# Performance work log

Hardware: AMD Instinct MI355X
Metric: run time of the kernel (lower is better)

The kernel has to match this reference:

```python
import jax, jax.numpy as jnp
import numpy as np

L, B, S, D, W = 3, 32, 512, 512, 3
EPS = 1e-6

def setup_inputs() -> dict:
    key = jax.random.key(0)
    ks = jax.random.split(key, 12)
    s = 1.0 / np.sqrt(D)
    def n(k, shape, scale=1.0):
        return jax.random.normal(k, shape, dtype=jnp.float32) * scale
    return {
        'x': n(ks[0], (B, S, D)),
        'fwd_pad': n(ks[1], (L, W, D), s),
        'bwd_pad': n(ks[2], (L, W, D), s),
        'fwd_w': n(ks[3], (L, W + 1)),
        'bwd_w': n(ks[4], (L, W + 1)),
        'fwd_w1': n(ks[5], (L, D, D), s),
        'fwd_b1': jnp.zeros((L, D), jnp.float32),
        'fwd_w2': n(ks[6], (L, D, D), s),
        'fwd_b2': jnp.zeros((L, D), jnp.float32),
        'fwd_g': jnp.ones((L, D), jnp.float32),
        'fwd_beta': jnp.zeros((L, D), jnp.float32),
        'bwd_w1': n(ks[7], (L, D, D), s),
        'bwd_b1': jnp.zeros((L, D), jnp.float32),
        'bwd_w2': n(ks[8], (L, D, D), s),
        'bwd_b2': jnp.zeros((L, D), jnp.float32),
        'bwd_g': jnp.ones((L, D), jnp.float32),
        'bwd_beta': jnp.zeros((L, D), jnp.float32),
    }

def _ln(y, g, b):
    # Annotated-transformer LayerNorm: a2*(x-mean)/(std+eps)+b2, unbiased std
    m = y.mean(-1, keepdims=True)
    sd = jnp.std(y, -1, keepdims=True, ddof=1)
    return g * (y - m) / (sd + EPS) + b

def _ffn(y, w1, b1, w2, b2):
    h = jax.nn.relu(jnp.einsum('bsd,de->bse', y, w1) + b1)
    return jnp.einsum('bse,ef->bsf', h, w2) + b2

def _wsum(padded, w, seq_len, offset):
    # weighted sum over a sliding window of width W+1 (dropout=0, eval mode)
    win = jnp.stack([padded[:, offset + k: offset + k + seq_len] for k in range(W + 1)], 0)
    return jnp.einsum('k,kbsd->bsd', w, win)

def reference(x, fwd_pad, bwd_pad, fwd_w, bwd_w,
              fwd_w1, fwd_b1, fwd_w2, fwd_b2, fwd_g, fwd_beta,
              bwd_w1, bwd_b1, bwd_w2, bwd_b2, bwd_g, bwd_beta):
    bsz, seq_len, _ = x.shape
    xf, xb = x, x
    outs = []
    for i in range(L):
        fp = jnp.broadcast_to(fwd_pad[i], (bsz, W, D))
        bp = jnp.broadcast_to(bwd_pad[i], (bsz, W, D))
        pf = jnp.concatenate([fp, xf, bp], axis=1)  # [B, S+2W, D]
        pb = jnp.concatenate([fp, xb, bp], axis=1)
        yf = _wsum(pf, fwd_w[i], seq_len, 0)       # windows [t, t+W]
        yb = _wsum(pb, bwd_w[i], seq_len, W)       # windows [t+W, t+2W]
        xf = yf + _ffn(_ln(yf, fwd_g[i], fwd_beta[i]), fwd_w1[i], fwd_b1[i], fwd_w2[i], fwd_b2[i])
        xb = yb + _ffn(_ln(yb, bwd_g[i], bwd_beta[i]), bwd_w1[i], bwd_b1[i], bwd_w2[i], bwd_b2[i])
        outs.append(jnp.concatenate([xf, xb], axis=-1))
    return jnp.stack(outs, 0)  # [L, B, S, 2D]
```

## Files before the change

### kernel.cpp

```cpp
#include <hip/hip_runtime.h>

#define S_LEN 512
#define D_DIM 512
#define BATCH 32
#define M_ROWS (BATCH * S_LEN)
#define NLAYER 3

typedef unsigned short ushort_t;
typedef __bf16 bf16_t;
typedef bf16_t bf16x8 __attribute__((ext_vector_type(8)));
typedef unsigned short u16x8 __attribute__((ext_vector_type(8)));
typedef float f32x4 __attribute__((ext_vector_type(4)));

typedef const __attribute__((address_space(1))) unsigned int* gptr_t;
typedef __attribute__((address_space(3))) unsigned int* lptr_t;

__device__ __forceinline__ ushort_t f2bf(float f) {
  unsigned u = __float_as_uint(f);
  unsigned r = (u + 0x7fffu + ((u >> 16) & 1u)) >> 16;
  return (ushort_t)r;
}

__global__ __launch_bounds__(256)
void wprep_kernel(const float* __restrict__ fw1, const float* __restrict__ fw2,
                  const float* __restrict__ bw1, const float* __restrict__ bw2,
                  ushort_t* __restrict__ wt1, ushort_t* __restrict__ wt2) {
  int z = blockIdx.z;
  int l = z >> 2, m = z & 3;
  const float* bases[4] = {fw1, fw2, bw1, bw2};
  const float* src = bases[m] + (size_t)l * D_DIM * D_DIM;
  int streamIdx = m >> 1;
  int which = m & 1;
  ushort_t* dst = (which ? wt2 : wt1) + ((size_t)streamIdx * NLAYER + l) * D_DIM * D_DIM;

  __shared__ float tile[32][33];
  int n0 = blockIdx.x * 32, k0 = blockIdx.y * 32;
  int tx = threadIdx.x, ty = threadIdx.y;
#pragma unroll
  for (int i = 0; i < 32; i += 8)
    tile[ty + i][tx] = src[(size_t)(k0 + ty + i) * D_DIM + n0 + tx];
  __syncthreads();
#pragma unroll
  for (int i = 0; i < 32; i += 8)
    dst[(size_t)(n0 + ty + i) * D_DIM + k0 + tx] = f2bf(tile[tx][ty + i]);
}

__global__ __launch_bounds__(256)
void conv_ln_kernel(const float* __restrict__ srcF, int strideF,
                    const float* __restrict__ srcB, int strideB,
                    const float* __restrict__ padLo, const float* __restrict__ padHi,
                    const float* __restrict__ wF, const float* __restrict__ wB,
                    const float* __restrict__ gF, const float* __restrict__ beF,
                    const float* __restrict__ gB, const float* __restrict__ beB,
                    ushort_t* __restrict__ yln) {
  int z = blockIdx.y;
  int tid = threadIdx.x;
  int lane = tid & 63;
  int rl = tid >> 6;
  int row = blockIdx.x * 4 + rl;
  int t = row & (S_LEN - 1);
  const float* src = z ? srcB : srcF;
  int stride = z ? strideB : strideF;
  const float* wv = z ? wB : wF;
  const float* gv = z ? gB : gF;
  const float* bv = z ? beB : beF;
  int toff = z ? 0 : -3;
  int c0 = lane * 4, c1 = 256 + lane * 4;

  float4 a0 = make_float4(0.f, 0.f, 0.f, 0.f);
  float4 a1 = make_float4(0.f, 0.f, 0.f, 0.f);
#pragma unroll
  for (int k = 0; k < 4; ++k) {
    int tt = t + k + toff;
    const float* rp;
    if (tt < 0)            rp = padLo + (size_t)(tt + 3) * D_DIM;
    else if (tt >= S_LEN)  rp = padHi + (size_t)(tt - S_LEN) * D_DIM;
    else                   rp = src + (size_t)(row + k + toff) * stride;
    float wk = wv[k];
    float4 u0 = *(const float4*)(rp + c0);
    float4 u1 = *(const float4*)(rp + c1);
    a0.x = fmaf(wk, u0.x, a0.x); a0.y = fmaf(wk, u0.y, a0.y);
    a0.z = fmaf(wk, u0.z, a0.z); a0.w = fmaf(wk, u0.w, a0.w);
    a1.x = fmaf(wk, u1.x, a1.x); a1.y = fmaf(wk, u1.y, a1.y);
    a1.z = fmaf(wk, u1.z, a1.z); a1.w = fmaf(wk, u1.w, a1.w);
  }
  float s = a0.x + a0.y + a0.z + a0.w + a1.x + a1.y + a1.z + a1.w;
#pragma unroll
  for (int o = 32; o; o >>= 1) s += __shfl_xor(s, o);
  float mean = s * (1.0f / 512.0f);
  float q = 0.f, dx;
  dx = a0.x - mean; q = fmaf(dx, dx, q);
  dx = a0.y - mean; q = fmaf(dx, dx, q);
  dx = a0.z - mean; q = fmaf(dx, dx, q);
  dx = a0.w - mean; q = fmaf(dx, dx, q);
  dx = a1.x - mean; q = fmaf(dx, dx, q);
  dx = a1.y - mean; q = fmaf(dx, dx, q);
  dx = a1.z - mean; q = fmaf(dx, dx, q);
  dx = a1.w - mean; q = fmaf(dx, dx, q);
#pragma unroll
  for (int o = 32; o; o >>= 1) q += __shfl_xor(q, o);
  float sd = sqrtf(q * (1.0f / 511.0f));
  float inv = 1.0f / (sd + 1e-6f);

  size_t base = ((size_t)z * M_ROWS + row) * D_DIM;
  float4 g0 = *(const float4*)(gv + c0), g1 = *(const float4*)(gv + c1);
  float4 b0 = *(const float4*)(bv + c0), b1 = *(const float4*)(bv + c1);
  ushort_t p0[4], p1[4];
  p0[0] = f2bf(g0.x * ((a0.x - mean) * inv) + b0.x);
  p0[1] = f2bf(g0.y * ((a0.y - mean) * inv) + b0.y);
  p0[2] = f2bf(g0.z * ((a0.z - mean) * inv) + b0.z);
  p0[3] = f2bf(g0.w * ((a0.w - mean) * inv) + b0.w);
  p1[0] = f2bf(g1.x * ((a1.x - mean) * inv) + b1.x);
  p1[1] = f2bf(g1.y * ((a1.y - mean) * inv) + b1.y);
  p1[2] = f2bf(g1.z * ((a1.z - mean) * inv) + b1.z);
  p1[3] = f2bf(g1.w * ((a1.w - mean) * inv) + b1.w);
  *(uint2*)(yln + base + c0) = *(uint2*)p0;
  *(uint2*)(yln + base + c1) = *(uint2*)p1;
}

template <int EPI>
__global__ __launch_bounds__(256)
void gemm_kernel(const ushort_t* __restrict__ A,
                 const ushort_t* __restrict__ Bt_f, const ushort_t* __restrict__ Bt_b,
                 const float* __restrict__ bias_f, const float* __restrict__ bias_b,
                 ushort_t* __restrict__ Hout,
                 float* __restrict__ Cout,
                 const float* __restrict__ srcF, const float* __restrict__ srcB,
                 int srcStride,
                 const float* __restrict__ padLo, const float* __restrict__ padHi,
                 const float* __restrict__ wF, const float* __restrict__ wB) {
  const int K = 512;
  int lin = blockIdx.x;
  int xcd = lin & 7;
  int slot = lin >> 3;
  int nblk = slot & 3;
  int G = xcd * 32 + (slot >> 2);
  int z = G >> 7;
  int mblk = G & 127;

  const ushort_t* Ab = A + (size_t)z * M_ROWS * K + (size_t)mblk * 128 * K;
  const ushort_t* Bb = (z ? Bt_b : Bt_f) + (size_t)nblk * 128 * K;

  __shared__ __attribute__((aligned(16))) ushort_t As[128 * 32];
  __shared__ __attribute__((aligned(16))) ushort_t Bs[128 * 32];

  int tid = threadIdx.x, lane = tid & 63, wave = tid >> 6;
  int wr = wave >> 1, wc = wave & 1;
  int lm = lane & 15, lq = lane >> 4;

  f32x4 acc[4][4] = {};

  for (int kb = 0; kb < 16; ++kb) {
    int k0 = kb * 32;
#pragma unroll
    for (int i = 0; i < 2; ++i) {
      int slot2 = i * 256 + tid;
      int row = slot2 >> 2, kc = slot2 & 3;
      const ushort_t* ga = Ab + (size_t)row * K + k0 + kc * 8;
      const ushort_t* gb = Bb + (size_t)row * K + k0 + kc * 8;
      __builtin_amdgcn_global_load_lds((gptr_t)(const void*)ga,
                                       (lptr_t)(void*)(As + slot2 * 8), 16, 0, 0);
      __builtin_amdgcn_global_load_lds((gptr_t)(const void*)gb,
                                       (lptr_t)(void*)(Bs + slot2 * 8), 16, 0, 0);
    }
    __syncthreads();
    bf16x8 a[4], b[4];
#pragma unroll
    for (int i = 0; i < 4; ++i) {
      union { u16x8 u; bf16x8 b; } ua, ub;
      ua.u = *(const u16x8*)&As[(wr * 64 + i * 16 + lm) * 32 + lq * 8];
      ub.u = *(const u16x8*)&Bs[(wc * 64 + i * 16 + lm) * 32 + lq * 8];
      a[i] = ua.b; b[i] = ub.b;
    }
#pragma unroll
    for (int i = 0; i < 4; ++i)
#pragma unroll
      for (int j = 0; j < 4; ++j)
        acc[i][j] = __builtin_amdgcn_mfma_f32_16x16x32_bf16(a[i], b[j], acc[i][j], 0, 0, 0);
    __syncthreads();
  }

  const float* bias = z ? bias_b : bias_f;
  if (EPI == 1) {
    ushort_t* Hb = Hout + (size_t)z * M_ROWS * 512;
#pragma unroll
    for (int i = 0; i < 4; ++i) {
      int mbase = mblk * 128 + wr * 64 + i * 16 + lq * 4;
#pragma unroll
      for (int j = 0; j < 4; ++j) {
        int n = nblk * 128 + wc * 64 + j * 16 + lm;
        float bvn = bias[n];
#pragma unroll
        for (int r = 0; r < 4; ++r) {
          float v = fmaxf(acc[i][j][r] + bvn, 0.0f);
          Hb[(size_t)(mbase + r) * 512 + n] = f2bf(v);
        }
      }
    }
  } else {
    const float* src = z ? srcB : srcF;
    const float* wv = z ? wB : wF;
    int toff = z ? 0 : -3;
    float w0 = wv[0], w1 = wv[1], w2 = wv[2], w3 = wv[3];
    float* Cb = Cout + (size_t)z * 512;
#pragma unroll
    for (int i = 0; i < 4; ++i) {
      int mbase = mblk * 128 + wr * 64 + i * 16 + lq * 4;
      int t0 = mbase & (S_LEN - 1);
      int rb = mbase - t0;
      const float* rp[7];
#pragma unroll
      for (int q = 0; q < 7; ++q) {
        int tt = t0 + toff + q;
        rp[q] = (tt < 0)       ? padLo + (size_t)(tt + 3) * D_DIM
              : (tt >= S_LEN)  ? padHi + (size_t)(tt - S_LEN) * D_DIM
                               : src + (size_t)(rb + tt) * srcStride;
      }
#pragma unroll
      for (int j = 0; j < 4; ++j) {
        int n = nblk * 128 + wc * 64 + j * 16 + lm;
        float v[7];
#pragma unroll
        for (int q = 0; q < 7; ++q) v[q] = rp[q][n];
        float bvn = bias[n];
#pragma unroll
        for (int r = 0; r < 4; ++r) {
          float y = w0 * v[r] + w1 * v[r + 1] + w2 * v[r + 2] + w3 * v[r + 3];
          Cb[(size_t)(mbase + r) * 1024 + n] = acc[i][j][r] + bvn + y;
        }
      }
    }
  }
}

extern "C" void kernel_launch(void* const* d_in, const int* in_sizes, int n_in,
                              void* d_out, int out_size, void* d_ws, size_t ws_size,
                              hipStream_t stream) {
  const float* x        = (const float*)d_in[0];
  const float* fwd_pad  = (const float*)d_in[1];
  const float* bwd_pad  = (const float*)d_in[2];
  const float* fwd_w    = (const float*)d_in[3];
  const float* bwd_w    = (const float*)d_in[4];
  const float* fwd_w1   = (const float*)d_in[5];
  const float* fwd_b1   = (const float*)d_in[6];
  const float* fwd_w2   = (const float*)d_in[7];
  const float* fwd_b2   = (const float*)d_in[8];
  const float* fwd_g    = (const float*)d_in[9];
  const float* fwd_beta = (const float*)d_in[10];
  const float* bwd_w1   = (const float*)d_in[11];
  const float* bwd_b1   = (const float*)d_in[12];
  const float* bwd_w2   = (const float*)d_in[13];
  const float* bwd_b2   = (const float*)d_in[14];
  const float* bwd_g    = (const float*)d_in[15];
  const float* bwd_beta = (const float*)d_in[16];
  float* out = (float*)d_out;

  const size_t WSZ = (size_t)D_DIM * D_DIM;
  ushort_t* wt1 = (ushort_t*)d_ws;
  ushort_t* wt2 = wt1 + 2 * NLAYER * WSZ;
  ushort_t* yln = wt2 + 2 * NLAYER * WSZ;
  ushort_t* h   = yln + (size_t)2 * M_ROWS * D_DIM;

  wprep_kernel<<<dim3(16, 16, 12), dim3(32, 8), 0, stream>>>(
      fwd_w1, fwd_w2, bwd_w1, bwd_w2, wt1, wt2);

  for (int l = 0; l < NLAYER; ++l) {
    const float *srcF, *srcB;
    int str;
    if (l == 0) {
      srcF = x; srcB = x; str = 512;
    } else {
      srcF = out + (size_t)(l - 1) * M_ROWS * 1024;
      srcB = srcF + 512;
      str = 1024;
    }
    const float* pLo = fwd_pad + (size_t)l * 3 * D_DIM;
    const float* pHi = bwd_pad + (size_t)l * 3 * D_DIM;

    conv_ln_kernel<<<dim3(M_ROWS / 4, 2), 256, 0, stream>>>(
        srcF, str, srcB, str, pLo, pHi,
        fwd_w + l * 4, bwd_w + l * 4,
        fwd_g + l * D_DIM, fwd_beta + l * D_DIM,
        bwd_g + l * D_DIM, bwd_beta + l * D_DIM,
        yln);

    gemm_kernel<1><<<1024, 256, 0, stream>>>(
        yln, wt1 + (size_t)l * WSZ, wt1 + (size_t)(NLAYER + l) * WSZ,
        fwd_b1 + l * D_DIM, bwd_b1 + l * D_DIM,
        h, nullptr,
        nullptr, nullptr, 0, nullptr, nullptr, nullptr, nullptr);

    gemm_kernel<2><<<1024, 256, 0, stream>>>(
        h, wt2 + (size_t)l * WSZ, wt2 + (size_t)(NLAYER + l) * WSZ,
        fwd_b2 + l * D_DIM, bwd_b2 + l * D_DIM,
        nullptr, out + (size_t)l * M_ROWS * 1024,
        srcF, srcB, str, pLo, pHi,
        fwd_w + l * 4, bwd_w + l * 4);
  }
}
```

Measured before the change: 518.7 us.

## Fuse FFN GEMMs into one kernel keeping hidden activations in LDS

Replaces the two separate GEMM launches (W1+ReLU writing H to global, then W2 with conv residual epilogue) with one MLP kernel. Each block owns 64 rows and processes the hidden dimension in 128-wide chunks, storing the ReLU output in XOR-swizzled shared memory and accumulating the second GEMM into registers. This removes the global round trip of the bf16 hidden tensor and one launch per layer. In exchange, tiles are smaller (64 rows), the A tile is reloaded four times, the grid drops to 512 blocks, and the 128-wide-per-wave output accumulator increases register pressure.

Result: slower. 641.1 us (+23.6%).

```diff
diff --git a/kernel.cpp b/kernel.cpp
--- a/kernel.cpp
+++ b/kernel.cpp
@@ -118,116 +118,154 @@
   *(uint2*)(yln + base + c1) = *(uint2*)p1;
 }
 
-template <int EPI>
-__global__ __launch_bounds__(256)
-void gemm_kernel(const ushort_t* __restrict__ A,
-                 const ushort_t* __restrict__ Bt_f, const ushort_t* __restrict__ Bt_b,
-                 const float* __restrict__ bias_f, const float* __restrict__ bias_b,
-                 ushort_t* __restrict__ Hout,
-                 float* __restrict__ Cout,
-                 const float* __restrict__ srcF, const float* __restrict__ srcB,
-                 int srcStride,
-                 const float* __restrict__ padLo, const float* __restrict__ padHi,
-                 const float* __restrict__ wF, const float* __restrict__ wB) {
-  const int K = 512;
-  int lin = blockIdx.x;
-  int xcd = lin & 7;
-  int slot = lin >> 3;
-  int nblk = slot & 3;
-  int G = xcd * 32 + (slot >> 2);
-  int z = G >> 7;
-  int mblk = G & 127;
-
-  const ushort_t* Ab = A + (size_t)z * M_ROWS * K + (size_t)mblk * 128 * K;
-  const ushort_t* Bb = (z ? Bt_b : Bt_f) + (size_t)nblk * 128 * K;
-
-  __shared__ __attribute__((aligned(16))) ushort_t As[128 * 32];
-  __shared__ __attribute__((aligned(16))) ushort_t Bs[128 * 32];
-
-  int tid = threadIdx.x, lane = tid & 63, wave = tid >> 6;
-  int wr = wave >> 1, wc = wave & 1;
+__global__ __launch_bounds__(256, 2)
+void mlp_kernel(const ushort_t* __restrict__ A,
+                const ushort_t* __restrict__ W1t_f, const ushort_t* __restrict__ W1t_b,
+                const ushort_t* __restrict__ W2t_f, const ushort_t* __restrict__ W2t_b,
+                const float* __restrict__ b1_f, const float* __restrict__ b1_b,
+                const float* __restrict__ b2_f, const float* __restrict__ b2_b,
+                float* __restrict__ Cout,
+                const float* __restrict__ srcF, const float* __restrict__ srcB,
+                int srcStride,
+                const float* __restrict__ padLo, const float* __restrict__ padHi,
+                const float* __restrict__ wF, const float* __restrict__ wB) {
+  int bid = blockIdx.x;
+  int z = bid & 1;
+  int mtile = bid >> 1;
+  int row0 = mtile * 64;
+
+  const ushort_t* Ab  = A + ((size_t)z * M_ROWS + row0) * 512;
+  const ushort_t* W1t = z ? W1t_b : W1t_f;
+  const ushort_t* W2t = z ? W2t_b : W2t_f;
+  const float* b1 = z ? b1_b : b1_f;
+  const float* b2 = z ? b2_b : b2_f;
+
+  __shared__ __attribute__((aligned(16))) ushort_t As[64 * 32];
+  __shared__ __attribute__((aligned(16))) ushort_t Ws[512 * 32];
+  __shared__ __attribute__((aligned(16))) ushort_t Hs[64 * 128];
+
+  int tid = threadIdx.x, lane = tid & 63, w = tid >> 6;
   int lm = lane & 15, lq = lane >> 4;
 
-  f32x4 acc[4][4] = {};
-
-  for (int kb = 0; kb < 16; ++kb) {
-    int k0 = kb * 32;
-#pragma unroll
-    for (int i = 0; i < 2; ++i) {
-      int slot2 = i * 256 + tid;
-      int row = slot2 >> 2, kc = slot2 & 3;
-      const ushort_t* ga = Ab + (size_t)row * K + k0 + kc * 8;
-      const ushort_t* gb = Bb + (size_t)row * K + k0 + kc * 8;
-      __builtin_amdgcn_global_load_lds((gptr_t)(const void*)ga,
-                                       (lptr_t)(void*)(As + slot2 * 8), 16, 0, 0);
-      __builtin_amdgcn_global_load_lds((gptr_t)(const void*)gb,
-                                       (lptr_t)(void*)(Bs + slot2 * 8), 16, 0, 0);
-    }
+  f32x4 oacc[4][8] = {};
+
+  for (int c = 0; c < 4; ++c) {
+    f32x4 hacc[4][2] = {};
+    for (int ks = 0; ks < 16; ++ks) {
+      int k0 = ks * 32;
+      {
+        int rowa = tid >> 2, ka = (tid & 3) * 8;
+        __builtin_amdgcn_global_load_lds(
+            (gptr_t)(const void*)(Ab + (size_t)rowa * 512 + k0 + ka),
+            (lptr_t)(void*)(As + tid * 8), 16, 0, 0);
+      }
+#pragma unroll
+      for (int u = 0; u < 2; ++u) {
+        int ch = u * 256 + tid;
+        int rw = ch >> 2, kw = (ch & 3) * 8;
+        __builtin_amdgcn_global_load_lds(
+            (gptr_t)(const void*)(W1t + (size_t)(c * 128 + rw) * 512 + k0 + kw),
+            (lptr_t)(void*)(Ws + ch * 8), 16, 0, 0);
+      }
+      __syncthreads();
+      bf16x8 a[4], b[2];
+#pragma unroll
+      for (int i = 0; i < 4; ++i) {
+        union { u16x8 u; bf16x8 b; } ua;
+        ua.u = *(const u16x8*)&As[(i * 16 + lm) * 32 + lq * 8];
+        a[i] = ua.b;
+      }
+#pragma unroll
+      for (int j = 0; j < 2; ++j) {
+        union { u16x8 u; bf16x8 b; } ub;
+        ub.u = *(const u16x8*)&Ws[(w * 32 + j * 16 + lm) * 32 + lq * 8];
+        b[j] = ub.b;
+      }
+#pragma unroll
+      for (int i = 0; i < 4; ++i)
+#pragma unroll
+        for (int j = 0; j < 2; ++j)
+          hacc[i][j] = __builtin_amdgcn_mfma_f32_16x16x32_bf16(a[i], b[j], hacc[i][j], 0, 0, 0);
+      __syncthreads();
+    }
+#pragma unroll
+    for (int i = 0; i < 4; ++i)
+#pragma unroll
+      for (int j = 0; j < 2; ++j) {
+        int col = w * 32 + j * 16 + lm;
+        float bv = b1[c * 128 + col];
+#pragma unroll
+        for (int r = 0; r < 4; ++r) {
+          int rowh = i * 16 + lq * 4 + r;
+          float v = fmaxf(hacc[i][j][r] + bv, 0.0f);
+          int q = (rowh * 256 + col * 2) ^ ((rowh & 7) << 4);
+          *(ushort_t*)((char*)Hs + q) = f2bf(v);
+        }
+      }
     __syncthreads();
-    bf16x8 a[4], b[4];
-#pragma unroll
-    for (int i = 0; i < 4; ++i) {
-      union { u16x8 u; bf16x8 b; } ua, ub;
-      ua.u = *(const u16x8*)&As[(wr * 64 + i * 16 + lm) * 32 + lq * 8];
-      ub.u = *(const u16x8*)&Bs[(wc * 64 + i * 16 + lm) * 32 + lq * 8];
-      a[i] = ua.b; b[i] = ub.b;
-    }
-#pragma unroll
-    for (int i = 0; i < 4; ++i)
-#pragma unroll
-      for (int j = 0; j < 4; ++j)
-        acc[i][j] = __builtin_amdgcn_mfma_f32_16x16x32_bf16(a[i], b[j], acc[i][j], 0, 0, 0);
-    __syncthreads();
+    for (int ks = 0; ks < 4; ++ks) {
+#pragma unroll
+      for (int u = 0; u < 8; ++u) {
+        int ch = u * 256 + tid;
+        int rw = ch >> 2, kw = (ch & 3) * 8;
+        __builtin_amdgcn_global_load_lds(
+            (gptr_t)(const void*)(W2t + (size_t)rw * 512 + c * 128 + ks * 32 + kw),
+            (lptr_t)(void*)(Ws + ch * 8), 16, 0, 0);
+      }
+      __syncthreads();
+      bf16x8 a[4], b[8];
+#pragma unroll
+      for (int i = 0; i < 4; ++i) {
+        int rowh = i * 16 + lm;
+        int q = (rowh * 256 + ks * 64 + lq * 16) ^ ((rowh & 7) << 4);
+        union { u16x8 u; bf16x8 b; } ua;
+        ua.u = *(const u16x8*)((const char*)Hs + q);
+        a[i] = ua.b;
+      }
+#pragma unroll
+      for (int j = 0; j < 8; ++j) {
+        union { u16x8 u; bf16x8 b; } ub;
+        ub.u = *(const u16x8*)&Ws[(w * 128 + j * 16 + lm) * 32 + lq * 8];
+        b[j] = ub.b;
+      }
+#pragma unroll
+      for (int i = 0; i < 4; ++i)
+#pragma unroll
+        for (int j = 0; j < 8; ++j)
+          oacc[i][j] = __builtin_amdgcn_mfma_f32_16x16x32_bf16(a[i], b[j], oacc[i][j], 0, 0, 0);
+      __syncthreads();
+    }
   }
 
-  const float* bias = z ? bias_b : bias_f;
-  if (EPI == 1) {
-    ushort_t* Hb = Hout + (size_t)z * M_ROWS * 512;
-#pragma unroll
-    for (int i = 0; i < 4; ++i) {
-      int mbase = mblk * 128 + wr * 64 + i * 16 + lq * 4;
-#pragma unroll
-      for (int j = 0; j < 4; ++j) {
-        int n = nblk * 128 + wc * 64 + j * 16 + lm;
-        float bvn = bias[n];
-#pragma unroll
-        for (int r = 0; r < 4; ++r) {
-          float v = fmaxf(acc[i][j][r] + bvn, 0.0f);
-          Hb[(size_t)(mbase + r) * 512 + n] = f2bf(v);
-        }
-      }
-    }
-  } else {
-    const float* src = z ? srcB : srcF;
-    const float* wv = z ? wB : wF;
-    int toff = z ? 0 : -3;
-    float w0 = wv[0], w1 = wv[1], w2 = wv[2], w3 = wv[3];
-    float* Cb = Cout + (size_t)z * 512;
-#pragma unroll
-    for (int i = 0; i < 4; ++i) {
-      int mbase = mblk * 128 + wr * 64 + i * 16 + lq * 4;
-      int t0 = mbase & (S_LEN - 1);
-      int rb = mbase - t0;
-      const float* rp[7];
-#pragma unroll
-      for (int q = 0; q < 7; ++q) {
-        int tt = t0 + toff + q;
-        rp[q] = (tt < 0)       ? padLo + (size_t)(tt + 3) * D_DIM
-              : (tt >= S_LEN)  ? padHi + (size_t)(tt - S_LEN) * D_DIM
-                               : src + (size_t)(rb + tt) * srcStride;
-      }
-#pragma unroll
-      for (int j = 0; j < 4; ++j) {
-        int n = nblk * 128 + wc * 64 + j * 16 + lm;
-        float v[7];
-#pragma unroll
-        for (int q = 0; q < 7; ++q) v[q] = rp[q][n];
-        float bvn = bias[n];
-#pragma unroll
-        for (int r = 0; r < 4; ++r) {
-          float y = w0 * v[r] + w1 * v[r + 1] + w2 * v[r + 2] + w3 * v[r + 3];
-          Cb[(size_t)(mbase + r) * 1024 + n] = acc[i][j][r] + bvn + y;
-        }
+  const float* src = z ? srcB : srcF;
+  const float* wv = z ? wB : wF;
+  int toff = z ? 0 : -3;
+  float w0 = wv[0], w1 = wv[1], w2 = wv[2], w3 = wv[3];
+  float* Cb = Cout + (size_t)z * 512;
+#pragma unroll
+  for (int i = 0; i < 4; ++i) {
+    int mbase = row0 + i * 16 + lq * 4;
+    int t0 = mbase & (S_LEN - 1);
+    int rb = mbase - t0;
+    const float* rp[7];
+#pragma unroll
+    for (int q = 0; q < 7; ++q) {
+      int tt = t0 + toff + q;
+      rp[q] = (tt < 0)       ? padLo + (size_t)(tt + 3) * D_DIM
+            : (tt >= S_LEN)  ? padHi + (size_t)(tt - S_LEN) * D_DIM
+                             : src + (size_t)(rb + tt) * srcStride;
+    }
+#pragma unroll
+    for (int j = 0; j < 8; ++j) {
+      int n = w * 128 + j * 16 + lm;
+      float v[7];
+#pragma unroll
+      for (int q = 0; q < 7; ++q) v[q] = rp[q][n];
+      float bvn = b2[n];
+#pragma unroll
+      for (int r = 0; r < 4; ++r) {
+        float y = w0 * v[r] + w1 * v[r + 1] + w2 * v[r + 2] + w3 * v[r + 3];
+        Cb[(size_t)(mbase + r) * 1024 + n] = oacc[i][j][r] + bvn + y;
       }
     }
   }
@@ -259,7 +297,6 @@
   ushort_t* wt1 = (ushort_t*)d_ws;
   ushort_t* wt2 = wt1 + 2 * NLAYER * WSZ;
   ushort_t* yln = wt2 + 2 * NLAYER * WSZ;
-  ushort_t* h   = yln + (size_t)2 * M_ROWS * D_DIM;
 
   wprep_kernel<<<dim3(16, 16, 12), dim3(32, 8), 0, stream>>>(
       fwd_w1, fwd_w2, bwd_w1, bwd_w2, wt1, wt2);
@@ -284,16 +321,13 @@
         bwd_g + l * D_DIM, bwd_beta + l * D_DIM,
         yln);
 
-    gemm_kernel<1><<<1024, 256, 0, stream>>>(
-        yln, wt1 + (size_t)l * WSZ, wt1 + (size_t)(NLAYER + l) * WSZ,
+    mlp_kernel<<<512, 256, 0, stream>>>(
+        yln,
+        wt1 + (size_t)l * WSZ, wt1 + (size_t)(NLAYER + l) * WSZ,
+        wt2 + (size_t)l * WSZ, wt2 + (size_t)(NLAYER + l) * WSZ,
         fwd_b1 + l * D_DIM, bwd_b1 + l * D_DIM,
-        h, nullptr,
-        nullptr, nullptr, 0, nullptr, nullptr, nullptr, nullptr);
-
-    gemm_kernel<2><<<1024, 256, 0, stream>>>(
-        h, wt2 + (size_t)l * WSZ, wt2 + (size_t)(NLAYER + l) * WSZ,
         fwd_b2 + l * D_DIM, bwd_b2 + l * D_DIM,
-        nullptr, out + (size_t)l * M_ROWS * 1024,
+        out + (size_t)l * M_ROWS * 1024,
         srcF, srcB, str, pLo, pHi,
         fwd_w + l * 4, bwd_w + l * 4);
   }
```

## Rewrite FFN GEMMs as 256x256 tiles with double-buffered swizzled LDS pipeline

Applied to the files above, without the earlier changes.

Replaces the 128x128, single-buffered GEMM with 256x256 tiles per 512-thread block, a K-step of 64, and double-buffered LDS. Global-to-LDS staging of later K slices is interleaved with MFMA phases, using s_setprio, explicit vmcnt waits and barriers. LDS rows use an XOR swizzle to avoid bank conflicts. This aims to hide load latency and raise MFMA utilisation and operand reuse, but the grid shrinks to 256 blocks, which leaves some CUs idle or underfilled on a 256-CU part, and register pressure rises.

After: 490.4 us. 5.5% less time.

```diff
diff --git a/kernel.cpp b/kernel.cpp
--- a/kernel.cpp
+++ b/kernel.cpp
@@ -118,81 +118,185 @@
   *(uint2*)(yln + base + c1) = *(uint2*)p1;
 }
 
+#define PHASE_PRE()                                         \
+  __builtin_amdgcn_sched_barrier(0);                        \
+  __builtin_amdgcn_s_barrier();                             \
+  asm volatile("s_waitcnt lgkmcnt(0)" ::: "memory");        \
+  __builtin_amdgcn_sched_barrier(0);                        \
+  __builtin_amdgcn_s_setprio(1);
+
+#define PHASE_PRE_NOLGKM()                                  \
+  __builtin_amdgcn_sched_barrier(0);                        \
+  __builtin_amdgcn_s_barrier();                             \
+  __builtin_amdgcn_s_setprio(1);
+
+#define PHASE_POST()                                        \
+  __builtin_amdgcn_s_setprio(0);                            \
+  __builtin_amdgcn_sched_barrier(0);                        \
+  __builtin_amdgcn_s_barrier();
+
+#define GROUP_END_CK4()                                     \
+  __builtin_amdgcn_s_setprio(0);                            \
+  __builtin_amdgcn_sched_barrier(0);                        \
+  asm volatile("s_waitcnt vmcnt(4)" ::: "memory");          \
+  __builtin_amdgcn_sched_barrier(0);                        \
+  __builtin_amdgcn_s_barrier();
+
+#define GROUP_END_CK0()                                     \
+  __builtin_amdgcn_s_setprio(0);                            \
+  __builtin_amdgcn_sched_barrier(0);                        \
+  asm volatile("s_waitcnt vmcnt(0)" ::: "memory");          \
+  __builtin_amdgcn_sched_barrier(0);                        \
+  __builtin_amdgcn_s_barrier();
+
+#define READ_A(MH)                                                        \
+  _Pragma("unroll")                                                       \
+  for (int m_ = 0; m_ < 4; ++m_) {                                        \
+    _Pragma("unroll")                                                     \
+    for (int kk_ = 0; kk_ < 2; ++kk_) {                                   \
+      int row_ = ((MH) * 4 + m_) * 32 + wr16lm;                           \
+      int idx_ = (row_ * 64 + kk_ * 32 + lq * 8) ^ ((row_ & 7) * 8);      \
+      union { u16x8 u; bf16x8 b; } t_;                                    \
+      t_.u = *(const u16x8*)&pa[idx_];                                    \
+      aF[kk_][m_] = t_.b;                                                 \
+    }                                                                     \
+  }
+
+#define READ_B(NH)                                                        \
+  _Pragma("unroll")                                                       \
+  for (int n_ = 0; n_ < 2; ++n_) {                                        \
+    _Pragma("unroll")                                                     \
+    for (int kk_ = 0; kk_ < 2; ++kk_) {                                   \
+      int row_ = ((NH) * 2 + n_) * 64 + wc16lm;                           \
+      int idx_ = (row_ * 64 + kk_ * 32 + lq * 8) ^ ((row_ & 7) * 8);      \
+      union { u16x8 u; bf16x8 b; } t_;                                    \
+      t_.u = *(const u16x8*)&pb[idx_];                                    \
+      bF[NH][kk_][n_] = t_.b;                                             \
+    }                                                                     \
+  }
+
+#define MFMA16(MH, NH)                                                    \
+  _Pragma("unroll")                                                       \
+  for (int kk_ = 0; kk_ < 2; ++kk_)                                       \
+    _Pragma("unroll")                                                     \
+    for (int m_ = 0; m_ < 4; ++m_)                                        \
+      _Pragma("unroll")                                                   \
+      for (int n_ = 0; n_ < 2; ++n_)                                      \
+        acc[(MH) * 4 + m_][(NH) * 2 + n_] =                               \
+            __builtin_amdgcn_mfma_f32_16x16x32_bf16(                      \
+                aF[kk_][m_], bF[NH][kk_][n_],                             \
+                acc[(MH) * 4 + m_][(NH) * 2 + n_], 0, 0, 0);
+
 template <int EPI>
-__global__ __launch_bounds__(256)
-void gemm_kernel(const ushort_t* __restrict__ A,
-                 const ushort_t* __restrict__ Bt_f, const ushort_t* __restrict__ Bt_b,
-                 const float* __restrict__ bias_f, const float* __restrict__ bias_b,
-                 ushort_t* __restrict__ Hout,
-                 float* __restrict__ Cout,
-                 const float* __restrict__ srcF, const float* __restrict__ srcB,
-                 int srcStride,
-                 const float* __restrict__ padLo, const float* __restrict__ padHi,
-                 const float* __restrict__ wF, const float* __restrict__ wB) {
+__global__ __launch_bounds__(512, 2)
+void gemm256_kernel(const ushort_t* __restrict__ A,
+                    const ushort_t* __restrict__ Bt_f, const ushort_t* __restrict__ Bt_b,
+                    const float* __restrict__ bias_f, const float* __restrict__ bias_b,
+                    ushort_t* __restrict__ Hout,
+                    float* __restrict__ Cout,
+                    const float* __restrict__ srcF, const float* __restrict__ srcB,
+                    int srcStride,
+                    const float* __restrict__ padLo, const float* __restrict__ padHi,
+                    const float* __restrict__ wF, const float* __restrict__ wB) {
   const int K = 512;
-  int lin = blockIdx.x;
-  int xcd = lin & 7;
-  int slot = lin >> 3;
-  int nblk = slot & 3;
-  int G = xcd * 32 + (slot >> 2);
+  int bid = blockIdx.x;
+  int G = (bid & 7) * 32 + (bid >> 3);
   int z = G >> 7;
-  int mblk = G & 127;
-
-  const ushort_t* Ab = A + (size_t)z * M_ROWS * K + (size_t)mblk * 128 * K;
-  const ushort_t* Bb = (z ? Bt_b : Bt_f) + (size_t)nblk * 128 * K;
-
-  __shared__ __attribute__((aligned(16))) ushort_t As[128 * 32];
-  __shared__ __attribute__((aligned(16))) ushort_t Bs[128 * 32];
+  int t2 = G & 127;
+  int mblk = t2 >> 1, nblk = t2 & 1;
+  int row0 = mblk * 256, n0 = nblk * 256;
+
+  const ushort_t* Ab = A + (size_t)z * M_ROWS * K + (size_t)row0 * K;
+  const ushort_t* Bb = (z ? Bt_b : Bt_f) + (size_t)n0 * K;
+
+  __shared__ __attribute__((aligned(16))) ushort_t As[2][256 * 64];
+  __shared__ __attribute__((aligned(16))) ushort_t Bs[2][256 * 64];
 
   int tid = threadIdx.x, lane = tid & 63, wave = tid >> 6;
-  int wr = wave >> 1, wc = wave & 1;
+  int wr = wave >> 2, wc = wave & 3;
   int lm = lane & 15, lq = lane >> 4;
-
-  f32x4 acc[4][4] = {};
-
-  for (int kb = 0; kb < 16; ++kb) {
-    int k0 = kb * 32;
-#pragma unroll
-    for (int i = 0; i < 2; ++i) {
-      int slot2 = i * 256 + tid;
-      int row = slot2 >> 2, kc = slot2 & 3;
-      const ushort_t* ga = Ab + (size_t)row * K + k0 + kc * 8;
-      const ushort_t* gb = Bb + (size_t)row * K + k0 + kc * 8;
-      __builtin_amdgcn_global_load_lds((gptr_t)(const void*)ga,
-                                       (lptr_t)(void*)(As + slot2 * 8), 16, 0, 0);
-      __builtin_amdgcn_global_load_lds((gptr_t)(const void*)gb,
-                                       (lptr_t)(void*)(Bs + slot2 * 8), 16, 0, 0);
+  int wr16lm = wr * 16 + lm;
+  int wc16lm = wc * 16 + lm;
+
+  auto STAGE = [&](const ushort_t* src, ushort_t* dstBase, int half, int g) {
+#pragma unroll
+    for (int u = 0; u < 2; ++u) {
+      int ch = u * 512 + tid;
+      int r = ch >> 3;
+      int cs = ((ch & 7) ^ (r & 7)) * 8;
+      __builtin_amdgcn_global_load_lds(
+          (gptr_t)(const void*)(src + (size_t)(half * 128 + r) * 512 + g * 64 + cs),
+          (lptr_t)(void*)(dstBase + (half * 128 + r) * 64 + (ch & 7) * 8), 16, 0, 0);
     }
-    __syncthreads();
-    bf16x8 a[4], b[4];
-#pragma unroll
-    for (int i = 0; i < 4; ++i) {
-      union { u16x8 u; bf16x8 b; } ua, ub;
-      ua.u = *(const u16x8*)&As[(wr * 64 + i * 16 + lm) * 32 + lq * 8];
-      ub.u = *(const u16x8*)&Bs[(wc * 64 + i * 16 + lm) * 32 + lq * 8];
-      a[i] = ua.b; b[i] = ub.b;
+  };
+
+  f32x4 acc[8][4] = {};
+  bf16x8 aF[2][4];
+  bf16x8 bF[2][2][2];
+
+  STAGE(Ab, &As[0][0], 0, 0);
+  STAGE(Bb, &Bs[0][0], 0, 0);
+  STAGE(Ab, &As[0][0], 1, 0);
+  STAGE(Bb, &Bs[0][0], 1, 0);
+  STAGE(Ab, &As[1][0], 0, 1);
+  STAGE(Bb, &Bs[1][0], 0, 1);
+  asm volatile("s_waitcnt vmcnt(4)" ::: "memory");
+  __builtin_amdgcn_sched_barrier(0);
+  __builtin_amdgcn_s_barrier();
+
+#pragma unroll
+  for (int g = 0; g < 8; ++g) {
+    const ushort_t* pa = &As[g & 1][0];
+    const ushort_t* pb = &Bs[g & 1][0];
+    ushort_t* oa = &As[(g & 1) ^ 1][0];
+    ushort_t* ob = &Bs[(g & 1) ^ 1][0];
+    ushort_t* ca = &As[g & 1][0];
+    ushort_t* cb = &Bs[g & 1][0];
+
+    READ_A(0)
+    READ_B(0)
+    if (g + 1 < 8) STAGE(Ab, oa, 1, g + 1);
+    PHASE_PRE()
+    MFMA16(0, 0)
+    PHASE_POST()
+
+    READ_B(1)
+    if (g + 1 < 8) STAGE(Bb, ob, 1, g + 1);
+    PHASE_PRE()
+    MFMA16(0, 1)
+    PHASE_POST()
+
+    READ_A(1)
+    if (g + 2 < 8) STAGE(Ab, ca, 0, g + 2);
+    PHASE_PRE()
+    MFMA16(1, 0)
+    PHASE_POST()
+
+    if (g + 2 < 8) STAGE(Bb, cb, 0, g + 2);
+    PHASE_PRE_NOLGKM()
+    MFMA16(1, 1)
+    if (g < 6) {
+      GROUP_END_CK4()
+    } else if (g == 6) {
+      GROUP_END_CK0()
+    } else {
+      PHASE_POST()
     }
-#pragma unroll
-    for (int i = 0; i < 4; ++i)
-#pragma unroll
-      for (int j = 0; j < 4; ++j)
-        acc[i][j] = __builtin_amdgcn_mfma_f32_16x16x32_bf16(a[i], b[j], acc[i][j], 0, 0, 0);
-    __syncthreads();
   }
 
   const float* bias = z ? bias_b : bias_f;
   if (EPI == 1) {
     ushort_t* Hb = Hout + (size_t)z * M_ROWS * 512;
 #pragma unroll
-    for (int i = 0; i < 4; ++i) {
-      int mbase = mblk * 128 + wr * 64 + i * 16 + lq * 4;
-#pragma unroll
-      for (int j = 0; j < 4; ++j) {
-        int n = nblk * 128 + wc * 64 + j * 16 + lm;
+    for (int mf = 0; mf < 8; ++mf) {
+      int mbase = row0 + (mf * 2 + wr) * 16 + lq * 4;
+#pragma unroll
+      for (int nf = 0; nf < 4; ++nf) {
+        int n = n0 + (nf * 4 + wc) * 16 + lm;
         float bvn = bias[n];
 #pragma unroll
         for (int r = 0; r < 4; ++r) {
-          float v = fmaxf(acc[i][j][r] + bvn, 0.0f);
+          float v = fmaxf(acc[mf][nf][r] + bvn, 0.0f);
           Hb[(size_t)(mbase + r) * 512 + n] = f2bf(v);
         }
       }
@@ -204,8 +308,8 @@
     float w0 = wv[0], w1 = wv[1], w2 = wv[2], w3 = wv[3];
     float* Cb = Cout + (size_t)z * 512;
 #pragma unroll
-    for (int i = 0; i < 4; ++i) {
-      int mbase = mblk * 128 + wr * 64 + i * 16 + lq * 4;
+    for (int mf = 0; mf < 8; ++mf) {
+      int mbase = row0 + (mf * 2 + wr) * 16 + lq * 4;
       int t0 = mbase & (S_LEN - 1);
       int rb = mbase - t0;
       const float* rp[7];
@@ -217,8 +321,8 @@
                                : src + (size_t)(rb + tt) * srcStride;
       }
 #pragma unroll
-      for (int j = 0; j < 4; ++j) {
-        int n = nblk * 128 + wc * 64 + j * 16 + lm;
+      for (int nf = 0; nf < 4; ++nf) {
+        int n = n0 + (nf * 4 + wc) * 16 + lm;
         float v[7];
 #pragma unroll
         for (int q = 0; q < 7; ++q) v[q] = rp[q][n];
@@ -226,7 +330,7 @@
 #pragma unroll
         for (int r = 0; r < 4; ++r) {
           float y = w0 * v[r] + w1 * v[r + 1] + w2 * v[r + 2] + w3 * v[r + 3];
-          Cb[(size_t)(mbase + r) * 1024 + n] = acc[i][j][r] + bvn + y;
+          Cb[(size_t)(mbase + r) * 1024 + n] = acc[mf][nf][r] + bvn + y;
         }
       }
     }
@@ -284,13 +388,13 @@
         bwd_g + l * D_DIM, bwd_beta + l * D_DIM,
         yln);
 
-    gemm_kernel<1><<<1024, 256, 0, stream>>>(
+    gemm256_kernel<1><<<256, 512, 0, stream>>>(
         yln, wt1 + (size_t)l * WSZ, wt1 + (size_t)(NLAYER + l) * WSZ,
         fwd_b1 + l * D_DIM, bwd_b1 + l * D_DIM,
         h, nullptr,
         nullptr, nullptr, 0, nullptr, nullptr, nullptr, nullptr);
 
-    gemm_kernel<2><<<1024, 256, 0, stream>>>(
+    gemm256_kernel<2><<<256, 512, 0, stream>>>(
         h, wt2 + (size_t)l * WSZ, wt2 + (size_t)(NLAYER + l) * WSZ,
         fwd_b2 + l * D_DIM, bwd_b2 + l * D_DIM,
         nullptr, out + (size_t)l * M_ROWS * 1024,
```
